# Kernel optimization log

Measured on AMD Instinct MI355X. Metric: run time of the kernel, lower is better.

Reference implementation:

```python
import jax, jax.numpy as jnp
import numpy as np

EPS = 1e-06
SOUND_SPEED = 343.0
SUBBAND_EDGES = [500.0, 2000.0, 8000.0]
IS_SOUND_IDX = 0
RHO_IDX = 1
NUM_CANDIDATES = 64


def setup_inputs() -> dict:
    key = jax.random.key(0)
    ks = jax.random.split(key, 6)
    B, T, F, S, D = 16, 2048, 1025, 4, NUM_CANDIDATES
    phase = jax.random.normal(ks[0], (B, 1, T, F), dtype=jnp.float32)
    comb = jax.random.normal(ks[1], (B, 2, T, F), dtype=jnp.float32)
    scalar = jax.random.normal(ks[2], (B, T, S), dtype=jnp.float32)
    scalar_observed_mask = jax.random.uniform(ks[3], (B, T, S), dtype=jnp.float32)
    scalar_reliable_mask = jax.random.uniform(ks[4], (B, T, S), dtype=jnp.float32)
    stpacc = jax.random.normal(ks[5], (B, 1, T, D), dtype=jnp.float32)
    # STFT bin centers up to 24 kHz
    frequencies_hz = (jnp.arange(F, dtype=jnp.float32) * (24000.0 / (F - 1)))
    spacing_grid_hz = jnp.linspace(50.0, 1000.0, D, dtype=jnp.float32)
    return {
        'phase': phase, 'comb': comb, 'scalar': scalar,
        'scalar_observed_mask': scalar_observed_mask,
        'scalar_reliable_mask': scalar_reliable_mask,
        'stpacc': stpacc, 'frequencies_hz': frequencies_hz,
        'spacing_grid_hz': spacing_grid_hz,
    }


def _periodicity_basis(freq, spacing):
    # [D, F]: raised-cosine comb pattern for each candidate spacing
    pattern = 0.5 * (1.0 + jnp.cos(2.0 * np.pi * (freq[None, :] / jnp.maximum(spacing[:, None], 1e-06))))
    return pattern / jnp.maximum(pattern.mean(axis=-1, keepdims=True), EPS)


def _subband_masks(freq):
    # static boundaries: [min(f)] + edges + [max(f)+1]; all bands nonempty for this grid
    bounds = [jnp.min(freq)] + [jnp.float32(e) for e in SUBBAND_EDGES] + [jnp.max(freq) + 1.0]
    masks = [((freq >= lo) & (freq < hi)).astype(freq.dtype) for lo, hi in zip(bounds[:-1], bounds[1:])]
    return jnp.stack(masks, axis=0)  # [S_band, F]


def reference(phase, comb, scalar, scalar_observed_mask, scalar_reliable_mask,
              stpacc, frequencies_hz, spacing_grid_hz):
    freq = frequencies_hz.astype(phase.dtype)
    log_mag = phase[:, 0, :, :]                 # [B,T,F]
    smooth_d1 = comb[:, 0, :, :]
    abs_d1 = jnp.abs(comb[:, 1, :, :])
    log_mag_centered = log_mag - jnp.mean(log_mag, axis=-1, keepdims=True)
    trough = jax.nn.relu(-log_mag_centered)
    d1_strength = jax.nn.relu(abs_d1) + 0.25 * jax.nn.relu(jnp.abs(smooth_d1))
    trough = trough * (1.0 + d1_strength)
    trough = trough / jnp.maximum(jnp.mean(trough, axis=-1, keepdims=True), EPS)

    basis = _periodicity_basis(freq, spacing_grid_hz.astype(phase.dtype))  # [D,F]
    D, F = basis.shape
    periodic_score = jnp.einsum('btf,df->btd', trough, basis) / float(F)

    channels = [periodic_score]
    bands = _subband_masks(freq)                           # [Sb,F]
    denom = jnp.maximum(jnp.sum(bands, axis=-1), 1.0)      # [Sb]
    masked_basis = basis[None, :, :] * bands[:, None, :]   # [Sb,D,F]
    band_scores = jnp.einsum('btf,sdf->bstd', trough, masked_basis) / denom[None, :, None, None]
    channels += [band_scores[:, s] for s in range(bands.shape[0])]

    # stpacc projection (last dim already == D, no interpolation needed)
    stp = jax.nn.relu(stpacc[:, 0, :, :])
    stp = stp / jnp.maximum(jnp.mean(stp, axis=-1, keepdims=True), EPS)
    channels.append(stp)

    B, T = trough.shape[0], trough.shape[1]
    obs_quality = jnp.broadcast_to(jnp.mean(scalar_observed_mask, axis=-1, keepdims=True), (B, T, D))
    rel_quality = jnp.broadcast_to(jnp.mean(scalar_reliable_mask, axis=-1, keepdims=True), (B, T, D))
    channels.append(obs_quality)
    channels.append(rel_quality)

    is_sound = jnp.broadcast_to(jnp.clip(scalar[:, :, IS_SOUND_IDX:IS_SOUND_IDX + 1], 0.0, 1.0), (B, T, D))
    channels.append(is_sound)
    rho = jnp.broadcast_to(jnp.abs(jnp.clip(scalar[:, :, RHO_IDX:RHO_IDX + 1], -1.0, 1.0)), (B, T, D))
    channels.append(rho)

    raw_likelihood_seq = jnp.stack(channels, axis=-1)      # [B,T,D,10]
    raw_distance_logits_seq = jnp.mean(raw_likelihood_seq, axis=-1) * (0.5 + 0.5 * is_sound)

    distance_grid_cm = (100.0 * SOUND_SPEED) / (2.0 * jnp.maximum(spacing_grid_hz, 1e-06))
    return (raw_likelihood_seq, raw_distance_logits_seq,
            spacing_grid_hz.astype(phase.dtype), distance_grid_cm.astype(phase.dtype))
```

## Files before the change

### kernel.cpp

```cpp
#include <hip/hip_runtime.h>
#include <hip/hip_fp16.h>
#include <math.h>

#define Bn 16
#define Tn 2048
#define Fn 1025
#define KP 1056
#define KROW 1064
#define ROWS 8
#define Dn 64
#define EPSF 1e-6f

typedef __attribute__((ext_vector_type(8))) _Float16 f16x8;
typedef __attribute__((ext_vector_type(4))) _Float16 f16x4;
typedef __attribute__((ext_vector_type(4))) float f32x4;

__device__ inline float waveReduceSum(float v) {
#pragma unroll
  for (int off = 32; off > 0; off >>= 1) v += __shfl_xor(v, off, 64);
  return v;
}

__global__ __launch_bounds__(256) void prep_kernel(
    const float* __restrict__ freq, const float* __restrict__ spacing,
    _Float16* __restrict__ basisT, float* __restrict__ out2, float* __restrict__ out3) {
  __shared__ float wsum[4];
  const int d = blockIdx.x;
  const int tid = threadIdx.x;
  const float sp = fmaxf(spacing[d], 1e-6f);

  float pv[5];
  float lsum = 0.f;
#pragma unroll
  for (int it = 0; it < 5; ++it) {
    int f = tid + 256 * it;
    float p = 0.f;
    if (f < Fn) {
      double arg = 6.2831853071795864769 * (double)(freq[f] / sp);
      p = 0.5f * (1.0f + (float)cos(arg));
      lsum += p;
    }
    pv[it] = p;
  }
  float s = waveReduceSum(lsum);
  if ((tid & 63) == 0) wsum[tid >> 6] = s;
  __syncthreads();
  float inv = 1.0f / fmaxf((wsum[0] + wsum[1] + wsum[2] + wsum[3]) * (1.0f / 1025.0f), EPSF);

#pragma unroll
  for (int it = 0; it < 5; ++it) {
    int f = tid + 256 * it;
    if (f < KP) basisT[(size_t)d * KP + f] = (_Float16)(pv[it] * inv);
  }
  if (tid == 0) {
    out2[d] = spacing[d];
    out3[d] = 17150.0f / sp;
  }
}

__global__ __launch_bounds__(256) void fused_kernel(
    const float* __restrict__ phase, const float* __restrict__ comb,
    const _Float16* __restrict__ basisT,
    const float* __restrict__ scalar, const float* __restrict__ obs_m,
    const float* __restrict__ rel_m, const float* __restrict__ stpacc,
    float* __restrict__ out0, float* __restrict__ out1) {
  __shared__ _Float16 uLDS[ROWS * KROW];
  __shared__ float rowScale[ROWS];

  const int lane = threadIdx.x & 63;
  const int w = __builtin_amdgcn_readfirstlane(threadIdx.x >> 6);
  const int row0 = blockIdx.x * ROWS;

#pragma unroll 1
  for (int k4 = 0; k4 < 2; ++k4) {
    const int rl = w * 2 + k4;
    const int row = row0 + rl;
    const int b = row >> 11;
    const int t = row & 2047;

    const float* prow  = phase + (size_t)row * Fn;
    const float* c0row = comb + ((size_t)(b * 2 + 0) * Tn + t) * Fn;
    const float* c1row = comb + ((size_t)(b * 2 + 1) * Tn + t) * Fn;

    float4 pv[5], c0v[5], c1v[5];
#pragma unroll
    for (int it = 0; it < 5; ++it) {
      const int i = lane + 64 * it;
      if (i < 256) {
        pv[it]  = *(const float4*)(prow  + 4 * i);
        c0v[it] = *(const float4*)(c0row + 4 * i);
        c1v[it] = *(const float4*)(c1row + 4 * i);
      } else if (i == 256) {
        pv[it]  = make_float4(prow[1024],  0.f, 0.f, 0.f);
        c0v[it] = make_float4(c0row[1024], 0.f, 0.f, 0.f);
        c1v[it] = make_float4(c1row[1024], 0.f, 0.f, 0.f);
      } else {
        pv[it]  = make_float4(0.f, 0.f, 0.f, 0.f);
        c0v[it] = make_float4(0.f, 0.f, 0.f, 0.f);
        c1v[it] = make_float4(0.f, 0.f, 0.f, 0.f);
      }
    }

    float s = 0.f;
#pragma unroll
    for (int it = 0; it < 5; ++it)
      s += pv[it].x + pv[it].y + pv[it].z + pv[it].w;
    s = waveReduceSum(s);
    const float mean_lm = s * (1.0f / 1025.0f);

    _Float16* urow = uLDS + (size_t)rl * KROW;
    float su = 0.f;
#pragma unroll
    for (int it = 0; it < 5; ++it) {
      const int i = lane + 64 * it;
      float4 u;
      const float* pf = (const float*)&pv[it];
      const float* q0 = (const float*)&c0v[it];
      const float* q1 = (const float*)&c1v[it];
      float* uf = (float*)&u;
#pragma unroll
      for (int c2 = 0; c2 < 4; ++c2) {
        float tr = fmaxf(mean_lm - pf[c2], 0.f);
        float d1 = fabsf(q1[c2]) + 0.25f * fabsf(q0[c2]);
        uf[c2] = tr * (1.f + d1);
      }
      if (i > 256) { u.x = 0.f; u.y = 0.f; u.z = 0.f; u.w = 0.f; }
      else if (i == 256) { u.y = 0.f; u.z = 0.f; u.w = 0.f; }
      su += u.x + u.y + u.z + u.w;
      if (i < 264) {
        f16x4 hv;
#pragma unroll
        for (int c2 = 0; c2 < 4; ++c2) hv[c2] = (_Float16)uf[c2];
        *(f16x4*)(urow + 4 * i) = hv;
      }
    }
    su = waveReduceSum(su);
    if (lane == 0) rowScale[rl] = 1.0f / fmaxf(su * (1.0f / 1025.0f), EPSF);
  }
  __syncthreads();

  const int m16 = lane & 15;
  const int kg = lane >> 4;
  const int nh = w & 1;
  const int kh = w >> 1;
  const int d0 = nh * 32 + m16;

  const _Float16* ALp = uLDS + (size_t)(m16 & 7) * KROW + kg * 8;
  const _Float16* B0 = basisT + (size_t)d0 * KP + kg * 8;
  const _Float16* B1 = basisT + (size_t)(d0 + 16) * KP + kg * 8;

  f32x4 acc0 = {0.f, 0.f, 0.f, 0.f};
  f32x4 acc1 = {0.f, 0.f, 0.f, 0.f};
  f32x4 s0a = acc0, s0b = acc0, s1a = acc0, s1b = acc0, s2a = acc0, s2b = acc0;

  auto loadA = [&](int kt) { return *(const f16x8*)(ALp + kt * 32); };
  auto tileA = [&](int kt, f16x8 a) {
    f16x8 b0 = *(const f16x8*)(B0 + kt * 32);
    f16x8 b1 = *(const f16x8*)(B1 + kt * 32);
    acc0 = __builtin_amdgcn_mfma_f32_16x16x32_f16(a, b0, acc0, 0, 0, 0);
    acc1 = __builtin_amdgcn_mfma_f32_16x16x32_f16(a, b1, acc1, 0, 0, 0);
  };
  auto boundary = [&](int kt, int KB, f32x4& sa, f32x4& sb) {
    f16x8 a = loadA(kt);
    const int kb = kt * 32 + kg * 8;
    f16x8 alo, ahi;
#pragma unroll
    for (int j = 0; j < 8; ++j) {
      bool lo = (kb + j) < KB;
      alo[j] = lo ? a[j] : (_Float16)0.f;
      ahi[j] = lo ? (_Float16)0.f : a[j];
    }
    tileA(kt, alo);
    sa = acc0; sb = acc1;
    tileA(kt, ahi);
  };

  if (kh == 0) {
    boundary(0, 22, s0a, s0b);
    tileA(1, loadA(1));
    boundary(2, 86, s1a, s1b);
#pragma unroll
    for (int kt = 3; kt < 10; ++kt) tileA(kt, loadA(kt));
    boundary(10, 342, s2a, s2b);
#pragma unroll
    for (int kt = 11; kt < 16; ++kt) tileA(kt, loadA(kt));
  } else {
#pragma unroll
    for (int kt = 16; kt < 33; ++kt) tileA(kt, loadA(kt));
  }
  __syncthreads();

  float* cumL = (float*)uLDS;
  auto stor = [&](int slot, const f32x4& v0, const f32x4& v1) {
    if (kg < 2) {
#pragma unroll
      for (int r = 0; r < 4; ++r) {
        const int rr = kg * 4 + r;
        cumL[(rr * 5 + slot) * 65 + d0]      = v0[r];
        cumL[(rr * 5 + slot) * 65 + d0 + 16] = v1[r];
      }
    }
  };
  if (kh == 0) {
    stor(0, s0a, s0b);
    stor(1, s1a, s1b);
    stor(2, s2a, s2b);
    stor(3, acc0, acc1);
  } else {
    stor(4, acc0, acc1);
  }
  __syncthreads();

#pragma unroll
  for (int k4 = 0; k4 < 2; ++k4) {
    const int rl = w * 2 + k4;
    const size_t bt = (size_t)(row0 + rl);
    const float rs = rowScale[rl];

    float q0 = cumL[(rl * 5 + 0) * 65 + lane];
    float q1 = cumL[(rl * 5 + 1) * 65 + lane];
    float q2 = cumL[(rl * 5 + 2) * 65 + lane];
    float q3 = cumL[(rl * 5 + 3) * 65 + lane] + cumL[(rl * 5 + 4) * 65 + lane];
    float b0 = q0, b1 = q1 - q0, b2 = q2 - q1, b3 = q3 - q2;

    float sv = fmaxf(stpacc[bt * Dn + lane], 0.f);
    float ssum = waveReduceSum(sv);
    float stp = sv / fmaxf(ssum * (1.0f / 64.0f), EPSF);

    float4 scv = *(const float4*)(scalar + bt * 4);
    float4 om  = *(const float4*)(obs_m  + bt * 4);
    float4 rm  = *(const float4*)(rel_m  + bt * 4);
    float obs_q = (om.x + om.y + om.z + om.w) * 0.25f;
    float rel_q = (rm.x + rm.y + rm.z + rm.w) * 0.25f;
    float is_snd = fminf(fmaxf(scv.x, 0.f), 1.f);
    float rho = fabsf(fminf(fmaxf(scv.y, -1.f), 1.f));

    float c0 = q3 * rs * (1.0f / 1025.0f);
    float c1 = b0 * rs * (1.0f / 22.0f);
    float c2 = b1 * rs * (1.0f / 64.0f);
    float c3 = b2 * rs * (1.0f / 256.0f);
    float c4 = b3 * rs * (1.0f / 683.0f);

    float mean10 = (c0 + c1 + c2 + c3 + c4 + stp + obs_q + rel_q + is_snd + rho) * 0.1f;
    float logit = mean10 * (0.5f + 0.5f * is_snd);

    float2* op = (float2*)(out0 + (bt * Dn + lane) * 10);
    op[0] = make_float2(c0, c1);
    op[1] = make_float2(c2, c3);
    op[2] = make_float2(c4, stp);
    op[3] = make_float2(obs_q, rel_q);
    op[4] = make_float2(is_snd, rho);
    out1[bt * Dn + lane] = logit;
  }
}

extern "C" void kernel_launch(void* const* d_in, const int* in_sizes, int n_in,
                              void* d_out, int out_size, void* d_ws, size_t ws_size,
                              hipStream_t stream) {
  const float* phase   = (const float*)d_in[0];
  const float* comb    = (const float*)d_in[1];
  const float* scalar  = (const float*)d_in[2];
  const float* obs_m   = (const float*)d_in[3];
  const float* rel_m   = (const float*)d_in[4];
  const float* stpacc  = (const float*)d_in[5];
  const float* freq    = (const float*)d_in[6];
  const float* spacing = (const float*)d_in[7];

  float* out  = (float*)d_out;
  float* out0 = out;
  float* out1 = out + (size_t)Bn * Tn * Dn * 10;
  float* out2 = out1 + (size_t)Bn * Tn * Dn;
  float* out3 = out2 + Dn;

  _Float16* basisT = (_Float16*)d_ws;

  prep_kernel<<<Dn, 256, 0, stream>>>(freq, spacing, basisT, out2, out3);
  fused_kernel<<<Bn * Tn / ROWS, 256, 0, stream>>>(
      phase, comb, basisT, scalar, obs_m, rel_m, stpacc, out0, out1);
}
```

Baseline: 131.3 us.

## Process 16 rows per block to fill MFMA M dimension and interleave row loads

```diff
diff --git a/kernel.cpp b/kernel.cpp
--- a/kernel.cpp
+++ b/kernel.cpp
@@ -7,7 +7,7 @@
 #define Fn 1025
 #define KP 1056
 #define KROW 1064
-#define ROWS 8
+#define ROWS 16
 #define Dn 64
 #define EPSF 1e-6f
 
@@ -19,6 +19,13 @@
 #pragma unroll
   for (int off = 32; off > 0; off >>= 1) v += __shfl_xor(v, off, 64);
   return v;
+}
+__device__ inline void waveReduceSum2(float& a, float& b) {
+#pragma unroll
+  for (int off = 32; off > 0; off >>= 1) {
+    a += __shfl_xor(a, off, 64);
+    b += __shfl_xor(b, off, 64);
+  }
 }
 
 __global__ __launch_bounds__(256) void prep_kernel(
@@ -58,7 +65,7 @@
   }
 }
 
-__global__ __launch_bounds__(256) void fused_kernel(
+__global__ __launch_bounds__(256, 3) void fused_kernel(
     const float* __restrict__ phase, const float* __restrict__ comb,
     const _Float16* __restrict__ basisT,
     const float* __restrict__ scalar, const float* __restrict__ obs_m,
@@ -71,18 +78,12 @@
   const int w = __builtin_amdgcn_readfirstlane(threadIdx.x >> 6);
   const int row0 = blockIdx.x * ROWS;
 
-#pragma unroll 1
-  for (int k4 = 0; k4 < 2; ++k4) {
-    const int rl = w * 2 + k4;
-    const int row = row0 + rl;
+  auto loadRow = [&](int row, float4* pv, float4* c0v, float4* c1v) {
     const int b = row >> 11;
     const int t = row & 2047;
-
     const float* prow  = phase + (size_t)row * Fn;
     const float* c0row = comb + ((size_t)(b * 2 + 0) * Tn + t) * Fn;
     const float* c1row = comb + ((size_t)(b * 2 + 1) * Tn + t) * Fn;
-
-    float4 pv[5], c0v[5], c1v[5];
 #pragma unroll
     for (int it = 0; it < 5; ++it) {
       const int i = lane + 64 * it;
@@ -100,14 +101,16 @@
         c1v[it] = make_float4(0.f, 0.f, 0.f, 0.f);
       }
     }
-
+  };
+  auto rowSum = [&](const float4* pv) {
     float s = 0.f;
 #pragma unroll
     for (int it = 0; it < 5; ++it)
       s += pv[it].x + pv[it].y + pv[it].z + pv[it].w;
-    s = waveReduceSum(s);
-    const float mean_lm = s * (1.0f / 1025.0f);
-
+    return s;
+  };
+  auto rowU = [&](int rl, float mean_lm, const float4* pv, const float4* c0v,
+                  const float4* c1v) {
     _Float16* urow = uLDS + (size_t)rl * KROW;
     float su = 0.f;
 #pragma unroll
@@ -134,8 +137,25 @@
         *(f16x4*)(urow + 4 * i) = hv;
       }
     }
-    su = waveReduceSum(su);
-    if (lane == 0) rowScale[rl] = 1.0f / fmaxf(su * (1.0f / 1025.0f), EPSF);
+    return su;
+  };
+
+#pragma unroll 1
+  for (int p = 0; p < 2; ++p) {
+    const int rA = w * 4 + p * 2;
+    const int rB = rA + 1;
+    float4 pvA[5], c0A[5], c1A[5], pvB[5], c0B[5], c1B[5];
+    loadRow(row0 + rA, pvA, c0A, c1A);
+    loadRow(row0 + rB, pvB, c0B, c1B);
+    float sA = rowSum(pvA), sB = rowSum(pvB);
+    waveReduceSum2(sA, sB);
+    float suA = rowU(rA, sA * (1.0f / 1025.0f), pvA, c0A, c1A);
+    float suB = rowU(rB, sB * (1.0f / 1025.0f), pvB, c0B, c1B);
+    waveReduceSum2(suA, suB);
+    if (lane == 0) {
+      rowScale[rA] = 1.0f / fmaxf(suA * (1.0f / 1025.0f), EPSF);
+      rowScale[rB] = 1.0f / fmaxf(suB * (1.0f / 1025.0f), EPSF);
+    }
   }
   __syncthreads();
 
@@ -145,7 +165,7 @@
   const int kh = w >> 1;
   const int d0 = nh * 32 + m16;
 
-  const _Float16* ALp = uLDS + (size_t)(m16 & 7) * KROW + kg * 8;
+  const _Float16* ALp = uLDS + (size_t)m16 * KROW + kg * 8;
   const _Float16* B0 = basisT + (size_t)d0 * KP + kg * 8;
   const _Float16* B1 = basisT + (size_t)(d0 + 16) * KP + kg * 8;
 
@@ -192,13 +212,11 @@
 
   float* cumL = (float*)uLDS;
   auto stor = [&](int slot, const f32x4& v0, const f32x4& v1) {
-    if (kg < 2) {
-#pragma unroll
-      for (int r = 0; r < 4; ++r) {
-        const int rr = kg * 4 + r;
-        cumL[(rr * 5 + slot) * 65 + d0]      = v0[r];
-        cumL[(rr * 5 + slot) * 65 + d0 + 16] = v1[r];
-      }
+#pragma unroll
+    for (int r = 0; r < 4; ++r) {
+      const int rr = kg * 4 + r;
+      cumL[(rr * 5 + slot) * 65 + d0]      = v0[r];
+      cumL[(rr * 5 + slot) * 65 + d0 + 16] = v1[r];
     }
   };
   if (kh == 0) {
@@ -212,10 +230,12 @@
   __syncthreads();
 
 #pragma unroll
-  for (int k4 = 0; k4 < 2; ++k4) {
-    const int rl = w * 2 + k4;
+  for (int k4 = 0; k4 < 4; ++k4) {
+    const int rl = w * 4 + k4;
     const size_t bt = (size_t)(row0 + rl);
     const float rs = rowScale[rl];
+
+    float sv = fmaxf(stpacc[bt * Dn + lane], 0.f);
 
     float q0 = cumL[(rl * 5 + 0) * 65 + lane];
     float q1 = cumL[(rl * 5 + 1) * 65 + lane];
@@ -223,7 +243,6 @@
     float q3 = cumL[(rl * 5 + 3) * 65 + lane] + cumL[(rl * 5 + 4) * 65 + lane];
     float b0 = q0, b1 = q1 - q0, b2 = q2 - q1, b3 = q3 - q2;
 
-    float sv = fmaxf(stpacc[bt * Dn + lane], 0.f);
     float ssum = waveReduceSum(sv);
     float stp = sv / fmaxf(ssum * (1.0f / 64.0f), EPSF);
 
```

After: 124.0 us. -5.5%, faster.

## Use 16-row blocks with 16 waves splitting K across eight partial-sum groups

Applied to the files above, without the earlier changes.

```diff
diff --git a/kernel.cpp b/kernel.cpp
--- a/kernel.cpp
+++ b/kernel.cpp
@@ -7,7 +7,8 @@
 #define Fn 1025
 #define KP 1056
 #define KROW 1064
-#define ROWS 8
+#define ROWS 16
+#define NSLOT 11
 #define Dn 64
 #define EPSF 1e-6f
 
@@ -58,26 +59,24 @@
   }
 }
 
-__global__ __launch_bounds__(256) void fused_kernel(
+__global__ __launch_bounds__(1024) void fused_kernel(
     const float* __restrict__ phase, const float* __restrict__ comb,
     const _Float16* __restrict__ basisT,
     const float* __restrict__ scalar, const float* __restrict__ obs_m,
     const float* __restrict__ rel_m, const float* __restrict__ stpacc,
     float* __restrict__ out0, float* __restrict__ out1) {
   __shared__ _Float16 uLDS[ROWS * KROW];
+  __shared__ float cumS[ROWS * NSLOT * 65];
   __shared__ float rowScale[ROWS];
 
   const int lane = threadIdx.x & 63;
   const int w = __builtin_amdgcn_readfirstlane(threadIdx.x >> 6);
   const int row0 = blockIdx.x * ROWS;
 
-#pragma unroll 1
-  for (int k4 = 0; k4 < 2; ++k4) {
-    const int rl = w * 2 + k4;
-    const int row = row0 + rl;
+  {
+    const int row = row0 + w;
     const int b = row >> 11;
     const int t = row & 2047;
-
     const float* prow  = phase + (size_t)row * Fn;
     const float* c0row = comb + ((size_t)(b * 2 + 0) * Tn + t) * Fn;
     const float* c1row = comb + ((size_t)(b * 2 + 1) * Tn + t) * Fn;
@@ -108,7 +107,7 @@
     s = waveReduceSum(s);
     const float mean_lm = s * (1.0f / 1025.0f);
 
-    _Float16* urow = uLDS + (size_t)rl * KROW;
+    _Float16* urow = uLDS + (size_t)w * KROW;
     float su = 0.f;
 #pragma unroll
     for (int it = 0; it < 5; ++it) {
@@ -135,7 +134,7 @@
       }
     }
     su = waveReduceSum(su);
-    if (lane == 0) rowScale[rl] = 1.0f / fmaxf(su * (1.0f / 1025.0f), EPSF);
+    if (lane == 0) rowScale[w] = 1.0f / fmaxf(su * (1.0f / 1025.0f), EPSF);
   }
   __syncthreads();
 
@@ -145,13 +144,12 @@
   const int kh = w >> 1;
   const int d0 = nh * 32 + m16;
 
-  const _Float16* ALp = uLDS + (size_t)(m16 & 7) * KROW + kg * 8;
+  const _Float16* ALp = uLDS + (size_t)m16 * KROW + kg * 8;
   const _Float16* B0 = basisT + (size_t)d0 * KP + kg * 8;
   const _Float16* B1 = basisT + (size_t)(d0 + 16) * KP + kg * 8;
 
   f32x4 acc0 = {0.f, 0.f, 0.f, 0.f};
   f32x4 acc1 = {0.f, 0.f, 0.f, 0.f};
-  f32x4 s0a = acc0, s0b = acc0, s1a = acc0, s1b = acc0, s2a = acc0, s2b = acc0;
 
   auto loadA = [&](int kt) { return *(const f16x8*)(ALp + kt * 32); };
   auto tileA = [&](int kt, f16x8 a) {
@@ -160,6 +158,14 @@
     acc0 = __builtin_amdgcn_mfma_f32_16x16x32_f16(a, b0, acc0, 0, 0, 0);
     acc1 = __builtin_amdgcn_mfma_f32_16x16x32_f16(a, b1, acc1, 0, 0, 0);
   };
+  auto stor = [&](int slot, const f32x4& v0, const f32x4& v1) {
+#pragma unroll
+    for (int r = 0; r < 4; ++r) {
+      const int rr = kg * 4 + r;
+      cumS[(rr * NSLOT + slot) * 65 + d0]      = v0[r];
+      cumS[(rr * NSLOT + slot) * 65 + d0 + 16] = v1[r];
+    }
+  };
   auto boundary = [&](int kt, int KB, f32x4& sa, f32x4& sb) {
     f16x8 a = loadA(kt);
     const int kb = kt * 32 + kg * 8;
@@ -176,54 +182,46 @@
   };
 
   if (kh == 0) {
+    f32x4 s0a = acc0, s0b = acc0, s1a = acc0, s1b = acc0;
     boundary(0, 22, s0a, s0b);
     tileA(1, loadA(1));
     boundary(2, 86, s1a, s1b);
-#pragma unroll
-    for (int kt = 3; kt < 10; ++kt) tileA(kt, loadA(kt));
+    tileA(3, loadA(3));
+    stor(0, acc0, acc1);
+    stor(8, s0a, s0b);
+    stor(9, s1a, s1b);
+  } else if (kh == 2) {
+    f32x4 s2a = acc0, s2b = acc0;
+    tileA(8, loadA(8));
+    tileA(9, loadA(9));
     boundary(10, 342, s2a, s2b);
-#pragma unroll
-    for (int kt = 11; kt < 16; ++kt) tileA(kt, loadA(kt));
+    tileA(11, loadA(11));
+    stor(2, acc0, acc1);
+    stor(10, s2a, s2b);
   } else {
-#pragma unroll
-    for (int kt = 16; kt < 33; ++kt) tileA(kt, loadA(kt));
+    const int kb = kh * 4;
+    const int ke = (kh == 7) ? 33 : kb + 4;
+#pragma unroll 4
+    for (int kt = kb; kt < ke; ++kt) tileA(kt, loadA(kt));
+    stor(kh, acc0, acc1);
   }
   __syncthreads();
 
-  float* cumL = (float*)uLDS;
-  auto stor = [&](int slot, const f32x4& v0, const f32x4& v1) {
-    if (kg < 2) {
-#pragma unroll
-      for (int r = 0; r < 4; ++r) {
-        const int rr = kg * 4 + r;
-        cumL[(rr * 5 + slot) * 65 + d0]      = v0[r];
-        cumL[(rr * 5 + slot) * 65 + d0 + 16] = v1[r];
-      }
-    }
-  };
-  if (kh == 0) {
-    stor(0, s0a, s0b);
-    stor(1, s1a, s1b);
-    stor(2, s2a, s2b);
-    stor(3, acc0, acc1);
-  } else {
-    stor(4, acc0, acc1);
-  }
-  __syncthreads();
-
-#pragma unroll
-  for (int k4 = 0; k4 < 2; ++k4) {
-    const int rl = w * 2 + k4;
+  {
+    const int rl = w;
     const size_t bt = (size_t)(row0 + rl);
     const float rs = rowScale[rl];
 
-    float q0 = cumL[(rl * 5 + 0) * 65 + lane];
-    float q1 = cumL[(rl * 5 + 1) * 65 + lane];
-    float q2 = cumL[(rl * 5 + 2) * 65 + lane];
-    float q3 = cumL[(rl * 5 + 3) * 65 + lane] + cumL[(rl * 5 + 4) * 65 + lane];
-    float b0 = q0, b1 = q1 - q0, b2 = q2 - q1, b3 = q3 - q2;
-
     float sv = fmaxf(stpacc[bt * Dn + lane], 0.f);
+
+    float q[NSLOT];
+#pragma unroll
+    for (int s2 = 0; s2 < NSLOT; ++s2)
+      q[s2] = cumS[(rl * NSLOT + s2) * 65 + lane];
+
+    float total = q[0] + q[1] + q[2] + q[3] + q[4] + q[5] + q[6] + q[7];
+    float cum342 = q[0] + q[1] + q[10];
+
     float ssum = waveReduceSum(sv);
     float stp = sv / fmaxf(ssum * (1.0f / 64.0f), EPSF);
 
@@ -235,11 +233,11 @@
     float is_snd = fminf(fmaxf(scv.x, 0.f), 1.f);
     float rho = fabsf(fminf(fmaxf(scv.y, -1.f), 1.f));
 
-    float c0 = q3 * rs * (1.0f / 1025.0f);
-    float c1 = b0 * rs * (1.0f / 22.0f);
-    float c2 = b1 * rs * (1.0f / 64.0f);
-    float c3 = b2 * rs * (1.0f / 256.0f);
-    float c4 = b3 * rs * (1.0f / 683.0f);
+    float c0 = total * rs * (1.0f / 1025.0f);
+    float c1 = q[8] * rs * (1.0f / 22.0f);
+    float c2 = (q[9] - q[8]) * rs * (1.0f / 64.0f);
+    float c3 = (cum342 - q[9]) * rs * (1.0f / 256.0f);
+    float c4 = (total - cum342) * rs * (1.0f / 683.0f);
 
     float mean10 = (c0 + c1 + c2 + c3 + c4 + stp + obs_q + rel_q + is_snd + rho) * 0.1f;
     float logit = mean10 * (0.5f + 0.5f * is_snd);
@@ -275,6 +273,6 @@
   _Float16* basisT = (_Float16*)d_ws;
 
   prep_kernel<<<Dn, 256, 0, stream>>>(freq, spacing, basisT, out2, out3);
-  fused_kernel<<<Bn * Tn / ROWS, 256, 0, stream>>>(
+  fused_kernel<<<Bn * Tn / ROWS, 1024, 0, stream>>>(
       phase, comb, basisT, scalar, obs_m, rel_m, stpacc, out0, out1);
 }
```

Measured after the change: 137.4 us. 4.6% more time.

## Persistent blocks with double-buffered async global-to-LDS staging across row tiles

Applied to the files above, without the earlier changes.

```diff
diff --git a/kernel.cpp b/kernel.cpp
--- a/kernel.cpp
+++ b/kernel.cpp
@@ -7,7 +7,9 @@
 #define Fn 1025
 #define KP 1056
 #define KROW 1064
-#define ROWS 8
+#define TR 4
+#define GRID 512
+#define NT 16
 #define Dn 64
 #define EPSF 1e-6f
 
@@ -19,6 +21,12 @@
 #pragma unroll
   for (int off = 32; off > 0; off >>= 1) v += __shfl_xor(v, off, 64);
   return v;
+}
+
+__device__ inline void gload16(const float* g, float* l) {
+  __builtin_amdgcn_global_load_lds(
+      (const __attribute__((address_space(1))) void*)(g),
+      (__attribute__((address_space(3))) void*)(l), 16, 0, 0);
 }
 
 __global__ __launch_bounds__(256) void prep_kernel(
@@ -64,166 +72,148 @@
     const float* __restrict__ scalar, const float* __restrict__ obs_m,
     const float* __restrict__ rel_m, const float* __restrict__ stpacc,
     float* __restrict__ out0, float* __restrict__ out1) {
-  __shared__ _Float16 uLDS[ROWS * KROW];
-  __shared__ float rowScale[ROWS];
+  __shared__ float rawS[2][3][TR][1024];
+  __shared__ _Float16 uLDS[TR * KROW];
+  __shared__ float cumS[TR * 5 * 65];
+  __shared__ float rowScale0[TR], rowScale1[TR];
 
   const int lane = threadIdx.x & 63;
   const int w = __builtin_amdgcn_readfirstlane(threadIdx.x >> 6);
-  const int row0 = blockIdx.x * ROWS;
-
-#pragma unroll 1
-  for (int k4 = 0; k4 < 2; ++k4) {
-    const int rl = w * 2 + k4;
-    const int row = row0 + rl;
-    const int b = row >> 11;
-    const int t = row & 2047;
-
-    const float* prow  = phase + (size_t)row * Fn;
-    const float* c0row = comb + ((size_t)(b * 2 + 0) * Tn + t) * Fn;
-    const float* c1row = comb + ((size_t)(b * 2 + 1) * Tn + t) * Fn;
-
-    float4 pv[5], c0v[5], c1v[5];
-#pragma unroll
-    for (int it = 0; it < 5; ++it) {
-      const int i = lane + 64 * it;
-      if (i < 256) {
-        pv[it]  = *(const float4*)(prow  + 4 * i);
-        c0v[it] = *(const float4*)(c0row + 4 * i);
-        c1v[it] = *(const float4*)(c1row + 4 * i);
-      } else if (i == 256) {
-        pv[it]  = make_float4(prow[1024],  0.f, 0.f, 0.f);
-        c0v[it] = make_float4(c0row[1024], 0.f, 0.f, 0.f);
-        c1v[it] = make_float4(c1row[1024], 0.f, 0.f, 0.f);
-      } else {
-        pv[it]  = make_float4(0.f, 0.f, 0.f, 0.f);
-        c0v[it] = make_float4(0.f, 0.f, 0.f, 0.f);
-        c1v[it] = make_float4(0.f, 0.f, 0.f, 0.f);
-      }
-    }
-
-    float s = 0.f;
-#pragma unroll
-    for (int it = 0; it < 5; ++it)
-      s += pv[it].x + pv[it].y + pv[it].z + pv[it].w;
-    s = waveReduceSum(s);
-    const float mean_lm = s * (1.0f / 1025.0f);
-
-    _Float16* urow = uLDS + (size_t)rl * KROW;
-    float su = 0.f;
-#pragma unroll
-    for (int it = 0; it < 5; ++it) {
-      const int i = lane + 64 * it;
-      float4 u;
-      const float* pf = (const float*)&pv[it];
-      const float* q0 = (const float*)&c0v[it];
-      const float* q1 = (const float*)&c1v[it];
-      float* uf = (float*)&u;
-#pragma unroll
-      for (int c2 = 0; c2 < 4; ++c2) {
-        float tr = fmaxf(mean_lm - pf[c2], 0.f);
-        float d1 = fabsf(q1[c2]) + 0.25f * fabsf(q0[c2]);
-        uf[c2] = tr * (1.f + d1);
-      }
-      if (i > 256) { u.x = 0.f; u.y = 0.f; u.z = 0.f; u.w = 0.f; }
-      else if (i == 256) { u.y = 0.f; u.z = 0.f; u.w = 0.f; }
-      su += u.x + u.y + u.z + u.w;
-      if (i < 264) {
-        f16x4 hv;
-#pragma unroll
-        for (int c2 = 0; c2 < 4; ++c2) hv[c2] = (_Float16)uf[c2];
-        *(f16x4*)(urow + 4 * i) = hv;
-      }
-    }
-    su = waveReduceSum(su);
-    if (lane == 0) rowScale[rl] = 1.0f / fmaxf(su * (1.0f / 1025.0f), EPSF);
-  }
-  __syncthreads();
+  const int tile0 = blockIdx.x * NT;
 
   const int m16 = lane & 15;
   const int kg = lane >> 4;
   const int nh = w & 1;
   const int kh = w >> 1;
   const int d0 = nh * 32 + m16;
-
-  const _Float16* ALp = uLDS + (size_t)(m16 & 7) * KROW + kg * 8;
+  const _Float16* ALp = uLDS + (size_t)(m16 & 3) * KROW + kg * 8;
   const _Float16* B0 = basisT + (size_t)d0 * KP + kg * 8;
   const _Float16* B1 = basisT + (size_t)(d0 + 16) * KP + kg * 8;
 
-  f32x4 acc0 = {0.f, 0.f, 0.f, 0.f};
-  f32x4 acc1 = {0.f, 0.f, 0.f, 0.f};
-  f32x4 s0a = acc0, s0b = acc0, s1a = acc0, s1b = acc0, s2a = acc0, s2b = acc0;
-
-  auto loadA = [&](int kt) { return *(const f16x8*)(ALp + kt * 32); };
-  auto tileA = [&](int kt, f16x8 a) {
-    f16x8 b0 = *(const f16x8*)(B0 + kt * 32);
-    f16x8 b1 = *(const f16x8*)(B1 + kt * 32);
-    acc0 = __builtin_amdgcn_mfma_f32_16x16x32_f16(a, b0, acc0, 0, 0, 0);
-    acc1 = __builtin_amdgcn_mfma_f32_16x16x32_f16(a, b1, acc1, 0, 0, 0);
+  auto STAGE = [&](int tile, int buf, float* tl) {
+    const int row = tile * TR + w;
+    const int b = row >> 11;
+    const int t = row & 2047;
+    const float* pr = phase + (size_t)row * Fn;
+    const float* c0 = comb + ((size_t)(b * 2 + 0) * Tn + t) * Fn;
+    const float* c1 = comb + ((size_t)(b * 2 + 1) * Tn + t) * Fn;
+#pragma unroll
+    for (int c = 0; c < 4; ++c) {
+      gload16(pr + (c * 64 + lane) * 4, &rawS[buf][0][w][c * 256]);
+      gload16(c0 + (c * 64 + lane) * 4, &rawS[buf][1][w][c * 256]);
+      gload16(c1 + (c * 64 + lane) * 4, &rawS[buf][2][w][c * 256]);
+    }
+    tl[0] = pr[1024]; tl[1] = c0[1024]; tl[2] = c1[1024];
   };
-  auto boundary = [&](int kt, int KB, f32x4& sa, f32x4& sb) {
-    f16x8 a = loadA(kt);
-    const int kb = kt * 32 + kg * 8;
-    f16x8 alo, ahi;
-#pragma unroll
-    for (int j = 0; j < 8; ++j) {
-      bool lo = (kb + j) < KB;
-      alo[j] = lo ? a[j] : (_Float16)0.f;
-      ahi[j] = lo ? (_Float16)0.f : a[j];
-    }
-    tileA(kt, alo);
-    sa = acc0; sb = acc1;
-    tileA(kt, ahi);
+
+  auto U = [&](int buf, const float* tl, float* rowScale) {
+    float4 pv[4], c0v[4], c1v[4];
+#pragma unroll
+    for (int it = 0; it < 4; ++it) {
+      pv[it]  = *(const float4*)&rawS[buf][0][w][(lane + 64 * it) * 4];
+      c0v[it] = *(const float4*)&rawS[buf][1][w][(lane + 64 * it) * 4];
+      c1v[it] = *(const float4*)&rawS[buf][2][w][(lane + 64 * it) * 4];
+    }
+    float s = (lane == 0) ? tl[0] : 0.f;
+#pragma unroll
+    for (int it = 0; it < 4; ++it)
+      s += pv[it].x + pv[it].y + pv[it].z + pv[it].w;
+    s = waveReduceSum(s);
+    const float mean_lm = s * (1.0f / 1025.0f);
+
+    _Float16* urow = uLDS + (size_t)w * KROW;
+    float su = 0.f;
+#pragma unroll
+    for (int it = 0; it < 4; ++it) {
+      const float* pf = (const float*)&pv[it];
+      const float* q0 = (const float*)&c0v[it];
+      const float* q1 = (const float*)&c1v[it];
+      f16x4 hv;
+#pragma unroll
+      for (int c2 = 0; c2 < 4; ++c2) {
+        float tr = fmaxf(mean_lm - pf[c2], 0.f);
+        float d1 = fabsf(q1[c2]) + 0.25f * fabsf(q0[c2]);
+        float u = tr * (1.f + d1);
+        su += u;
+        hv[c2] = (_Float16)u;
+      }
+      *(f16x4*)(urow + (lane + 64 * it) * 4) = hv;
+    }
+    float u1024 = fmaxf(mean_lm - tl[0], 0.f) * (1.f + fabsf(tl[2]) + 0.25f * fabsf(tl[1]));
+    if (lane == 0) su += u1024;
+    if (lane < 32) urow[1024 + lane] = (lane == 0) ? (_Float16)u1024 : (_Float16)0.f;
+    su = waveReduceSum(su);
+    if (lane == 0) rowScale[w] = 1.0f / fmaxf(su * (1.0f / 1025.0f), EPSF);
   };
 
-  if (kh == 0) {
-    boundary(0, 22, s0a, s0b);
-    tileA(1, loadA(1));
-    boundary(2, 86, s1a, s1b);
-#pragma unroll
-    for (int kt = 3; kt < 10; ++kt) tileA(kt, loadA(kt));
-    boundary(10, 342, s2a, s2b);
-#pragma unroll
-    for (int kt = 11; kt < 16; ++kt) tileA(kt, loadA(kt));
-  } else {
-#pragma unroll
-    for (int kt = 16; kt < 33; ++kt) tileA(kt, loadA(kt));
-  }
-  __syncthreads();
-
-  float* cumL = (float*)uLDS;
-  auto stor = [&](int slot, const f32x4& v0, const f32x4& v1) {
-    if (kg < 2) {
-#pragma unroll
-      for (int r = 0; r < 4; ++r) {
-        const int rr = kg * 4 + r;
-        cumL[(rr * 5 + slot) * 65 + d0]      = v0[r];
-        cumL[(rr * 5 + slot) * 65 + d0 + 16] = v1[r];
+  auto MFMAphase = [&]() {
+    f32x4 acc0 = {0.f, 0.f, 0.f, 0.f};
+    f32x4 acc1 = {0.f, 0.f, 0.f, 0.f};
+    f32x4 s0a = acc0, s0b = acc0, s1a = acc0, s1b = acc0, s2a = acc0, s2b = acc0;
+
+    auto loadA = [&](int kt) { return *(const f16x8*)(ALp + kt * 32); };
+    auto tileA = [&](int kt, f16x8 a) {
+      f16x8 b0 = *(const f16x8*)(B0 + kt * 32);
+      f16x8 b1 = *(const f16x8*)(B1 + kt * 32);
+      acc0 = __builtin_amdgcn_mfma_f32_16x16x32_f16(a, b0, acc0, 0, 0, 0);
+      acc1 = __builtin_amdgcn_mfma_f32_16x16x32_f16(a, b1, acc1, 0, 0, 0);
+    };
+    auto boundary = [&](int kt, int KB, f32x4& sa, f32x4& sb) {
+      f16x8 a = loadA(kt);
+      const int kb = kt * 32 + kg * 8;
+      f16x8 alo, ahi;
+#pragma unroll
+      for (int j = 0; j < 8; ++j) {
+        bool lo = (kb + j) < KB;
+        alo[j] = lo ? a[j] : (_Float16)0.f;
+        ahi[j] = lo ? (_Float16)0.f : a[j];
       }
+      tileA(kt, alo);
+      sa = acc0; sb = acc1;
+      tileA(kt, ahi);
+    };
+    auto stor = [&](int slot, const f32x4& v0, const f32x4& v1) {
+      if (kg == 0) {
+#pragma unroll
+        for (int r = 0; r < 4; ++r) {
+          cumS[(r * 5 + slot) * 65 + d0]      = v0[r];
+          cumS[(r * 5 + slot) * 65 + d0 + 16] = v1[r];
+        }
+      }
+    };
+
+    if (kh == 0) {
+      boundary(0, 22, s0a, s0b);
+      tileA(1, loadA(1));
+      boundary(2, 86, s1a, s1b);
+#pragma unroll
+      for (int kt = 3; kt < 10; ++kt) tileA(kt, loadA(kt));
+      boundary(10, 342, s2a, s2b);
+#pragma unroll
+      for (int kt = 11; kt < 16; ++kt) tileA(kt, loadA(kt));
+      stor(0, s0a, s0b);
+      stor(1, s1a, s1b);
+      stor(2, s2a, s2b);
+      stor(3, acc0, acc1);
+    } else {
+#pragma unroll
+      for (int kt = 16; kt < 33; ++kt) tileA(kt, loadA(kt));
+      stor(4, acc0, acc1);
     }
   };
-  if (kh == 0) {
-    stor(0, s0a, s0b);
-    stor(1, s1a, s1b);
-    stor(2, s2a, s2b);
-    stor(3, acc0, acc1);
-  } else {
-    stor(4, acc0, acc1);
-  }
-  __syncthreads();
-
-#pragma unroll
-  for (int k4 = 0; k4 < 2; ++k4) {
-    const int rl = w * 2 + k4;
-    const size_t bt = (size_t)(row0 + rl);
-    const float rs = rowScale[rl];
-
-    float q0 = cumL[(rl * 5 + 0) * 65 + lane];
-    float q1 = cumL[(rl * 5 + 1) * 65 + lane];
-    float q2 = cumL[(rl * 5 + 2) * 65 + lane];
-    float q3 = cumL[(rl * 5 + 3) * 65 + lane] + cumL[(rl * 5 + 4) * 65 + lane];
+
+  auto EPI = [&](int tile, const float* rowScale) {
+    const size_t bt = (size_t)(tile * TR + w);
+    const float rs = rowScale[w];
+
+    float sv = fmaxf(stpacc[bt * Dn + lane], 0.f);
+
+    float q0 = cumS[(w * 5 + 0) * 65 + lane];
+    float q1 = cumS[(w * 5 + 1) * 65 + lane];
+    float q2 = cumS[(w * 5 + 2) * 65 + lane];
+    float q3 = cumS[(w * 5 + 3) * 65 + lane] + cumS[(w * 5 + 4) * 65 + lane];
     float b0 = q0, b1 = q1 - q0, b2 = q2 - q1, b3 = q3 - q2;
 
-    float sv = fmaxf(stpacc[bt * Dn + lane], 0.f);
     float ssum = waveReduceSum(sv);
     float stp = sv / fmaxf(ssum * (1.0f / 64.0f), EPSF);
 
@@ -251,7 +241,43 @@
     op[3] = make_float2(obs_q, rel_q);
     op[4] = make_float2(is_snd, rho);
     out1[bt * Dn + lane] = logit;
+  };
+
+  float tA[3], tB[3];
+
+  STAGE(tile0 + 0, 0, tA);
+  STAGE(tile0 + 1, 1, tB);
+  asm volatile("s_waitcnt vmcnt(15)" ::: "memory");
+  __builtin_amdgcn_sched_barrier(0);
+  U(0, tA, rowScale0);
+  asm volatile("s_waitcnt lgkmcnt(0)" ::: "memory");
+  __builtin_amdgcn_s_barrier();
+
+#define BODY(I, TS, TU, BS, BU, RSU, RSE)                       \
+  MFMAphase();                                                   \
+  STAGE(tile0 + ((I) + 2) % NT, BS, TS);                         \
+  asm volatile("s_waitcnt lgkmcnt(0)" ::: "memory");             \
+  __builtin_amdgcn_s_barrier();                                  \
+  asm volatile("s_waitcnt vmcnt(15)" ::: "memory");              \
+  __builtin_amdgcn_sched_barrier(0);                             \
+  U(BU, TU, RSU);                                                \
+  EPI(tile0 + (I), RSE);                                         \
+  asm volatile("s_waitcnt lgkmcnt(0)" ::: "memory");             \
+  __builtin_amdgcn_s_barrier();
+
+#pragma unroll 1
+  for (int ii = 0; ii < NT - 2; ii += 2) {
+    BODY(ii,     tA, tB, 0, 1, rowScale1, rowScale0)
+    BODY(ii + 1, tB, tA, 1, 0, rowScale0, rowScale1)
   }
+  BODY(NT - 2, tA, tB, 0, 1, rowScale1, rowScale0)
+#undef BODY
+
+  MFMAphase();
+  asm volatile("s_waitcnt lgkmcnt(0)" ::: "memory");
+  __builtin_amdgcn_s_barrier();
+  asm volatile("s_waitcnt vmcnt(0)" ::: "memory");
+  EPI(tile0 + NT - 1, rowScale1);
 }
 
 extern "C" void kernel_launch(void* const* d_in, const int* in_sizes, int n_in,
@@ -275,6 +301,6 @@
   _Float16* basisT = (_Float16*)d_ws;
 
   prep_kernel<<<Dn, 256, 0, stream>>>(freq, spacing, basisT, out2, out3);
-  fused_kernel<<<Bn * Tn / ROWS, 256, 0, stream>>>(
+  fused_kernel<<<GRID, 256, 0, stream>>>(
       phase, comb, basisT, scalar, obs_m, rel_m, stpacc, out0, out1);
 }
```

Result: slower. 185.6 us (+41.3%).
